# Performance work log

Hardware: AMD Instinct MI355X
Metric: run time of the kernel (lower is better)

Reference implementation:

```python
import jax, jax.numpy as jnp
import numpy as np

T, N, F_IN, H, E, OUT = 24, 20000, 64, 256, 320000, 1


def setup_inputs() -> dict:
    key = jax.random.key(0)
    ks = jax.random.split(key, 16)
    inp = {
        "x": jax.random.normal(ks[0], (T, N, F_IN), dtype=jnp.float32),
        "edge_index": jax.random.randint(ks[1], (2, E), 0, N, dtype=jnp.int32),
        "edge_weight": jax.random.uniform(ks[2], (E,), dtype=jnp.float32),
        # GCNConv 1 (input_size -> hidden)
        "W1": jax.random.normal(ks[3], (F_IN, H), dtype=jnp.float32) / np.sqrt(F_IN),
        "b1": jnp.zeros((H,), dtype=jnp.float32),
        # GCNConv 2 (hidden -> hidden)
        "W2": jax.random.normal(ks[4], (H, H), dtype=jnp.float32) / np.sqrt(H),
        "b2": jnp.zeros((H,), dtype=jnp.float32),
        # LayerNorm affine
        "ln_w": jnp.ones((H,), dtype=jnp.float32),
        "ln_b": jnp.zeros((H,), dtype=jnp.float32),
        # GRU (1 layer): weight_ih [3H,H_in], weight_hh [3H,H]
        "Wih": jax.random.normal(ks[5], (3 * H, H), dtype=jnp.float32) / np.sqrt(H),
        "Whh": jax.random.normal(ks[6], (3 * H, H), dtype=jnp.float32) / np.sqrt(H),
        "bih": jnp.zeros((3 * H,), dtype=jnp.float32),
        "bhh": jnp.zeros((3 * H,), dtype=jnp.float32),
        # fc
        "Wfc": jax.random.normal(ks[7], (OUT, H), dtype=jnp.float32) / np.sqrt(H),
        "bfc": jnp.zeros((OUT,), dtype=jnp.float32),
    }
    return inp


def _gcn_norm(edge_index, edge_weight, n_nodes):
    # PyG gcn_norm with self-loops (fill=1.0) and symmetric normalization.
    loop = jnp.arange(n_nodes, dtype=edge_index.dtype)
    src = jnp.concatenate([edge_index[0], loop])
    dst = jnp.concatenate([edge_index[1], loop])
    ew = jnp.concatenate([edge_weight, jnp.ones((n_nodes,), edge_weight.dtype)])
    deg = jax.ops.segment_sum(ew, dst, num_segments=n_nodes)
    dinv = jnp.where(deg > 0, jax.lax.rsqrt(deg), 0.0)
    norm = dinv[src] * ew * dinv[dst]
    return src, dst, norm


def _gcn_conv(x, src, dst, norm, W, b, n_nodes):
    h = x @ W                              # [N, out]
    msg = norm[:, None] * h[src]           # [E+N, out]
    out = jax.ops.segment_sum(msg, dst, num_segments=n_nodes)
    return out + b


def reference(x, edge_index, edge_weight, W1, b1, W2, b2, ln_w, ln_b,
              Wih, Whh, bih, bhh, Wfc, bfc):
    n_nodes = x.shape[1]
    src, dst, norm = _gcn_norm(edge_index, edge_weight, n_nodes)

    def encode(xt):  # xt: [N, F_IN]
        h = _gcn_conv(xt, src, dst, norm, W1, b1, n_nodes)
        h = jnp.where(h >= 0, h, 0.01 * h)  # leaky_relu, slope 0.01
        h = _gcn_conv(h, src, dst, norm, W2, b2, n_nodes)
        mu = jnp.mean(h, axis=-1, keepdims=True)
        var = jnp.mean(jnp.square(h - mu), axis=-1, keepdims=True)
        return (h - mu) * jax.lax.rsqrt(var + 1e-5) * ln_w + ln_b

    seq = jax.vmap(encode)(x)  # [T, N, H]

    def gru_step(h, xt):
        gi = xt @ Wih.T + bih
        gh = h @ Whh.T + bhh
        ir, iz, inn = jnp.split(gi, 3, axis=-1)
        hr, hz, hn = jnp.split(gh, 3, axis=-1)
        r = jax.nn.sigmoid(ir + hr)
        z = jax.nn.sigmoid(iz + hz)
        n = jnp.tanh(inn + r * hn)
        h_new = (1.0 - z) * n + z * h
        return h_new, None

    h0 = jnp.zeros((n_nodes, Whh.shape[1]), dtype=x.dtype)
    h_last, _ = jax.lax.scan(gru_step, h0, seq)
    return h_last @ Wfc.T + bfc  # [N, OUT]
```

## Files before the change

kernel.cpp:

```cpp
#include <hip/hip_runtime.h>
#include <math.h>

#define T_STEPS 24
#define N_NODES 20000
#define F_IN 64
#define H_DIM 256
#define H3 (3 * H_DIM)
#define TC 4
#define NCHUNK (T_STEPS / TC)

using f16x8 = __attribute__((ext_vector_type(8))) _Float16;
using f16x4 = __attribute__((ext_vector_type(4))) _Float16;
using f16x2 = __attribute__((ext_vector_type(2))) _Float16;
using f32x4 = __attribute__((ext_vector_type(4))) float;

__device__ __forceinline__ void gload_lds16(const void* g, void* l) {
    __builtin_amdgcn_global_load_lds(
        (const __attribute__((address_space(1))) void*)(uintptr_t)g,
        (__attribute__((address_space(3))) void*)l, 16, 0, 0);
}

__device__ __forceinline__ float sigmoidf_(float x) { return 1.0f / (1.0f + expf(-x)); }

__global__ void init_deg_kernel(float* deg, int* indeg, int n) {
    int i = blockIdx.x * blockDim.x + threadIdx.x;
    if (i < n) { deg[i] = 1.0f; indeg[i] = 0; }
}

__global__ void accum_deg_kernel(const int* __restrict__ src, const int* __restrict__ dst,
                                 const float* __restrict__ ew, float* deg, int* indeg, int E) {
    int e = blockIdx.x * blockDim.x + threadIdx.x;
    if (e < E) {
        atomicAdd(&deg[dst[e]], ew[e]);
        atomicAdd(&indeg[dst[e]], 1);
    }
}

__global__ void dinv_kernel(float* deg, float* selfnorm, int n) {
    int i = blockIdx.x * blockDim.x + threadIdx.x;
    if (i < n) {
        float d = deg[i];
        float di = (d > 0.0f) ? rsqrtf(d) : 0.0f;
        deg[i] = di;
        selfnorm[i] = di * di;
    }
}

__global__ void edge_norm_kernel(const int* __restrict__ src, const int* __restrict__ dst,
                                 const float* __restrict__ ew, const float* __restrict__ dinv,
                                 float* norm, int E) {
    int e = blockIdx.x * blockDim.x + threadIdx.x;
    if (e < E) norm[e] = dinv[src[e]] * ew[e] * dinv[dst[e]];
}

__global__ void scan_kernel(const int* __restrict__ indeg, int* offs, int* cursor, int N) {
    __shared__ int part[1024];
    int t = threadIdx.x;
    const int CH = (N + 1023) / 1024;
    int s = 0;
    for (int i = 0; i < CH; i++) {
        int idx = t * CH + i;
        if (idx < N) s += indeg[idx];
    }
    part[t] = s;
    __syncthreads();
    for (int off = 1; off < 1024; off <<= 1) {
        int v = (t >= off) ? part[t - off] : 0;
        __syncthreads();
        part[t] += v;
        __syncthreads();
    }
    int base = (t == 0) ? 0 : part[t - 1];
    for (int i = 0; i < CH; i++) {
        int idx = t * CH + i;
        if (idx < N) {
            offs[idx] = base;
            cursor[idx] = base;
            base += indeg[idx];
        }
    }
    if (t == 0) offs[N] = part[1023];
}

__global__ void csr_fill_kernel(const int* __restrict__ src, const int* __restrict__ dst,
                                const float* __restrict__ norm, int* cursor,
                                int* csr_src, float* csr_norm, int E) {
    int e = blockIdx.x * blockDim.x + threadIdx.x;
    if (e < E) {
        int d = dst[e];
        int pos = atomicAdd(&cursor[d], 1);
        csr_src[pos] = src[e];
        csr_norm[pos] = norm[e];
    }
}

__global__ void pack_b16_kernel(const float* __restrict__ W, _Float16* __restrict__ P,
                                int K, int Nn, int trans) {
    int idx = blockIdx.x * blockDim.x + threadIdx.x;
    int total = (K >> 3) * Nn;
    if (idx >= total) return;
    int kk = idx / Nn, c = idx - kk * Nn;
    int n = c;
    if (trans == 2) {
        int a = c / 48, w = c % 48;
        int g = w >> 4, b = w & 15;
        n = g * 256 + a * 16 + b;
    }
    size_t o = (size_t)idx * 8;
    for (int j = 0; j < 8; ++j) {
        float v = (trans != 0) ? W[(size_t)n * K + kk * 8 + j] : W[(size_t)(kk * 8 + j) * Nn + n];
        P[o + j] = (_Float16)v;
    }
}

__global__ void perm_bias_kernel(const float* __restrict__ b, float* __restrict__ pb) {
    int c = blockIdx.x * blockDim.x + threadIdx.x;
    if (c < H3) {
        int a = c / 48, w = c % 48;
        int g = w >> 4, bb = w & 15;
        pb[c] = b[g * 256 + a * 16 + bb];
    }
}

__global__ void agg1_kernel(const float* __restrict__ xs, const int* __restrict__ offs,
                            const int* __restrict__ csr_src, const float* __restrict__ csr_norm,
                            const float* __restrict__ selfnorm,
                            _Float16* __restrict__ out, int N) {
    int t = blockIdx.y;
    int n = blockIdx.x * 4 + (threadIdx.x >> 6);
    int lane = threadIdx.x & 63;
    int fg = lane & 15, ep = lane >> 4;
    const float* xsl = xs + (size_t)t * N * F_IN;
    f32x4 acc = (f32x4){0.f, 0.f, 0.f, 0.f};
    int e0 = offs[n], e1 = offs[n + 1];
    int e = e0 + ep;
    for (; e + 4 < e1; e += 8) {
        int sA = csr_src[e], sB = csr_src[e + 4];
        float wA = csr_norm[e], wB = csr_norm[e + 4];
        f32x4 vA = *(const f32x4*)&xsl[(size_t)sA * F_IN + fg * 4];
        f32x4 vB = *(const f32x4*)&xsl[(size_t)sB * F_IN + fg * 4];
#pragma unroll
        for (int c = 0; c < 4; ++c) acc[c] = fmaf(wA, vA[c], acc[c]);
#pragma unroll
        for (int c = 0; c < 4; ++c) acc[c] = fmaf(wB, vB[c], acc[c]);
    }
    if (e < e1) {
        int s = csr_src[e];
        float w = csr_norm[e];
        f32x4 v = *(const f32x4*)&xsl[(size_t)s * F_IN + fg * 4];
#pragma unroll
        for (int c = 0; c < 4; ++c) acc[c] = fmaf(w, v[c], acc[c]);
    }
#pragma unroll
    for (int c = 0; c < 4; ++c) {
        acc[c] += __shfl_xor(acc[c], 16, 64);
        acc[c] += __shfl_xor(acc[c], 32, 64);
    }
    f32x4 own = *(const f32x4*)&xsl[(size_t)n * F_IN + fg * 4];
    float sn = selfnorm[n];
#pragma unroll
    for (int c = 0; c < 4; ++c) acc[c] = fmaf(sn, own[c], acc[c]);
    if (ep == 0) {
        f16x4 o = { (_Float16)acc[0], (_Float16)acc[1], (_Float16)acc[2], (_Float16)acc[3] };
        *(f16x4*)&out[((size_t)t * N + n) * F_IN + fg * 4] = o;
    }
}

__global__ void agg2_kernel(const _Float16* __restrict__ hs, const int* __restrict__ offs,
                            const int* __restrict__ csr_src, const float* __restrict__ csr_norm,
                            const float* __restrict__ selfnorm,
                            _Float16* __restrict__ out, int N) {
    int t = blockIdx.y;
    int n = blockIdx.x * 4 + (threadIdx.x >> 6);
    int lane = threadIdx.x & 63;
    const _Float16* hsl = hs + (size_t)t * N * H_DIM;
    f16x4 own = *(const f16x4*)&hsl[(size_t)n * H_DIM + lane * 4];
    float sn = selfnorm[n];
    f32x4 acc;
#pragma unroll
    for (int c = 0; c < 4; ++c) acc[c] = sn * (float)own[c];
    int e0 = offs[n], e1 = offs[n + 1];
    int e = e0;
    for (; e + 4 <= e1; e += 4) {
        int s0 = csr_src[e], s1 = csr_src[e + 1], s2 = csr_src[e + 2], s3 = csr_src[e + 3];
        float w0 = csr_norm[e], w1 = csr_norm[e + 1], w2 = csr_norm[e + 2], w3 = csr_norm[e + 3];
        f16x4 v0 = *(const f16x4*)&hsl[(size_t)s0 * H_DIM + lane * 4];
        f16x4 v1 = *(const f16x4*)&hsl[(size_t)s1 * H_DIM + lane * 4];
        f16x4 v2 = *(const f16x4*)&hsl[(size_t)s2 * H_DIM + lane * 4];
        f16x4 v3 = *(const f16x4*)&hsl[(size_t)s3 * H_DIM + lane * 4];
#pragma unroll
        for (int c = 0; c < 4; ++c) acc[c] = fmaf(w0, (float)v0[c], acc[c]);
#pragma unroll
        for (int c = 0; c < 4; ++c) acc[c] = fmaf(w1, (float)v1[c], acc[c]);
#pragma unroll
        for (int c = 0; c < 4; ++c) acc[c] = fmaf(w2, (float)v2[c], acc[c]);
#pragma unroll
        for (int c = 0; c < 4; ++c) acc[c] = fmaf(w3, (float)v3[c], acc[c]);
    }
    for (; e < e1; ++e) {
        int s = csr_src[e];
        float w = csr_norm[e];
        f16x4 v = *(const f16x4*)&hsl[(size_t)s * H_DIM + lane * 4];
#pragma unroll
        for (int c = 0; c < 4; ++c) acc[c] = fmaf(w, (float)v[c], acc[c]);
    }
    f16x4 o = { (_Float16)acc[0], (_Float16)acc[1], (_Float16)acc[2], (_Float16)acc[3] };
    *(f16x4*)&out[((size_t)t * N + n) * H_DIM + lane * 4] = o;
}

__global__ __launch_bounds__(256, 4)
void conv1_kernel(const _Float16* __restrict__ A, const _Float16* __restrict__ Bp,
                  const float* __restrict__ bias, _Float16* __restrict__ C16,
                  int M, int Nn, int K) {
    __shared__ _Float16 As[4][128][8];
    __shared__ _Float16 Bs[4][128][8];

    const int tid = threadIdx.x;
    const int wave = tid >> 6, lane = tid & 63;
    const int bm = blockIdx.x * 128, bn = blockIdx.y * 128;
    const int wm = (wave >> 1) * 64, wn = (wave & 1) * 64;
    const int kq = lane >> 4, r = lane & 15;

    f32x4 acc[4][4];
#pragma unroll
    for (int i = 0; i < 4; ++i)
#pragma unroll
        for (int j = 0; j < 4; ++j) acc[i][j] = (f32x4){0.f, 0.f, 0.f, 0.f};

    for (int k0 = 0; k0 < K; k0 += 32) {
        __syncthreads();
        const int kb = k0 >> 3;
#pragma unroll
        for (int it = 0; it < 2; ++it) {
            int c = it * 256 + tid;
            int kk = c >> 7, idx = c & 127;
            int row = bm + idx;
            if (row >= M) row = M - 1;
            size_t aoff = (size_t)row * K + k0 + kk * 8;
            size_t boff = ((size_t)(kb + kk) * Nn + bn + idx) * 8;
            gload_lds16(A + aoff, &As[0][0][0] + (size_t)c * 8);
            gload_lds16(Bp + boff, &Bs[0][0][0] + (size_t)c * 8);
        }
        __syncthreads();

        f16x8 a[4], b[4];
#pragma unroll
        for (int f = 0; f < 4; ++f) {
            a[f] = *(const f16x8*)&As[kq][wm + f * 16 + r][0];
            b[f] = *(const f16x8*)&Bs[kq][wn + f * 16 + r][0];
        }
#pragma unroll
        for (int i = 0; i < 4; ++i)
#pragma unroll
            for (int j = 0; j < 4; ++j)
                acc[i][j] = __builtin_amdgcn_mfma_f32_16x16x32_f16(a[i], b[j], acc[i][j], 0, 0, 0);
    }

#pragma unroll
    for (int j = 0; j < 4; ++j) {
        int col = bn + wn + j * 16 + r;
        float bv = bias[col];
#pragma unroll
        for (int i = 0; i < 4; ++i) {
#pragma unroll
            for (int q = 0; q < 4; ++q) {
                int row = bm + wm + i * 16 + kq * 4 + q;
                if (row < M) {
                    float v = acc[i][j][q] + bv;
                    v = (v >= 0.0f) ? v : 0.01f * v;
                    C16[(size_t)row * Nn + col] = (_Float16)v;
                }
            }
        }
    }
}

__global__ __launch_bounds__(256, 2)
void conv2ln_kernel(const _Float16* __restrict__ A, const _Float16* __restrict__ Bp,
                    const float* __restrict__ b2, const float* __restrict__ lnw,
                    const float* __restrict__ lnb, _Float16* __restrict__ out, int M) {
    __shared__ _Float16 As[4][128][8];
    __shared__ _Float16 Bs[4][256][8];
    __shared__ float lnP[128][2][2];

    const int tid = threadIdx.x;
    const int wave = tid >> 6, lane = tid & 63;
    const int bm = blockIdx.x * 128;
    const int wm = (wave >> 1) * 64, wn = (wave & 1) * 128;
    const int cw = wave & 1;
    const int kq = lane >> 4, r = lane & 15;

    f32x4 acc[4][8];
#pragma unroll
    for (int i = 0; i < 4; ++i)
#pragma unroll
        for (int j = 0; j < 8; ++j) acc[i][j] = (f32x4){0.f, 0.f, 0.f, 0.f};

    for (int k0 = 0; k0 < H_DIM; k0 += 32) {
        __syncthreads();
        const int kb = k0 >> 3;
#pragma unroll
        for (int it = 0; it < 2; ++it) {
            int c = it * 256 + tid;
            int kk = c >> 7, idx = c & 127;
            int row = bm + idx;
            if (row >= M) row = M - 1;
            gload_lds16(A + (size_t)row * H_DIM + k0 + kk * 8, &As[0][0][0] + (size_t)c * 8);
        }
#pragma unroll
        for (int it = 0; it < 4; ++it) {
            int c = it * 256 + tid;
            int kk = c >> 8, col = c & 255;
            gload_lds16(Bp + ((size_t)(kb + kk) * H_DIM + col) * 8, &Bs[0][0][0] + (size_t)c * 8);
        }
        __syncthreads();

        f16x8 a[4], b[8];
#pragma unroll
        for (int f = 0; f < 4; ++f) a[f] = *(const f16x8*)&As[kq][wm + f * 16 + r][0];
#pragma unroll
        for (int f = 0; f < 8; ++f) b[f] = *(const f16x8*)&Bs[kq][wn + f * 16 + r][0];
#pragma unroll
        for (int i = 0; i < 4; ++i)
#pragma unroll
            for (int j = 0; j < 8; ++j)
                acc[i][j] = __builtin_amdgcn_mfma_f32_16x16x32_f16(a[i], b[j], acc[i][j], 0, 0, 0);
    }

#pragma unroll
    for (int i = 0; i < 4; ++i) {
#pragma unroll
        for (int q = 0; q < 4; ++q) {
            float s = 0.f, s2 = 0.f;
#pragma unroll
            for (int j = 0; j < 8; ++j) {
                float v = acc[i][j][q] + b2[wn + j * 16 + r];
                acc[i][j][q] = v;
                s += v;
                s2 += v * v;
            }
#pragma unroll
            for (int m = 1; m < 16; m <<= 1) {
                s += __shfl_xor(s, m, 64);
                s2 += __shfl_xor(s2, m, 64);
            }
            int lrow = wm + i * 16 + kq * 4 + q;
            if (r == 0) { lnP[lrow][cw][0] = s; lnP[lrow][cw][1] = s2; }
        }
    }
    __syncthreads();

#pragma unroll
    for (int i = 0; i < 4; ++i) {
#pragma unroll
        for (int q = 0; q < 4; ++q) {
            int lrow = wm + i * 16 + kq * 4 + q;
            int row = bm + lrow;
            float S = lnP[lrow][0][0] + lnP[lrow][1][0];
            float S2 = lnP[lrow][0][1] + lnP[lrow][1][1];
            float mu = S * (1.0f / H_DIM);
            float var = S2 * (1.0f / H_DIM) - mu * mu;
            float rstd = rsqrtf(var + 1e-5f);
            if (row < M) {
#pragma unroll
                for (int j = 0; j < 8; ++j) {
                    int col = wn + j * 16 + r;
                    float o = (acc[i][j][q] - mu) * rstd * lnw[col] + lnb[col];
                    out[(size_t)row * H_DIM + col] = (_Float16)o;
                }
            }
        }
    }
}

__global__ __launch_bounds__(256, 2)
void gru_step_kernel(const _Float16* __restrict__ hprev, const _Float16* __restrict__ e,
                     const _Float16* __restrict__ Bhh, const _Float16* __restrict__ Bih,
                     const float* __restrict__ pbhh, const float* __restrict__ pbih,
                     _Float16* __restrict__ hnew, int M) {
    __shared__ _Float16 Ah[4][128][8];
    __shared__ _Float16 Ae[4][128][8];
    __shared__ _Float16 Bsh[4][96][8];
    __shared__ _Float16 Bsi[4][96][8];

    const int tid = threadIdx.x;
    const int wave = tid >> 6, lane = tid & 63;
    const int bm = blockIdx.y * 128, bn = blockIdx.x * 96;
    const int wm = (wave >> 1) * 64, wn = (wave & 1) * 48;
    const int kq = lane >> 4, r = lane & 15;

    f32x4 arz[4][2], ahn[4], ainn[4];
#pragma unroll
    for (int i = 0; i < 4; ++i) {
        arz[i][0] = (f32x4){0.f, 0.f, 0.f, 0.f};
        arz[i][1] = (f32x4){0.f, 0.f, 0.f, 0.f};
        ahn[i] = (f32x4){0.f, 0.f, 0.f, 0.f};
        ainn[i] = (f32x4){0.f, 0.f, 0.f, 0.f};
    }

    for (int k0 = 0; k0 < H_DIM; k0 += 32) {
        __syncthreads();
        const int kb = k0 >> 3;
#pragma unroll
        for (int it = 0; it < 2; ++it) {
            int c = it * 256 + tid;
            int kk = c >> 7, idx = c & 127;
            int row = bm + idx;
            if (row >= M) row = M - 1;
            size_t ao = (size_t)row * H_DIM + k0 + kk * 8;
            gload_lds16(hprev + ao, &Ah[0][0][0] + (size_t)c * 8);
            gload_lds16(e + ao, &Ae[0][0][0] + (size_t)c * 8);
        }
        {
            int c = tid;
            int kk = c / 96, col = c - kk * 96;
            size_t bo = ((size_t)(kb + kk) * H3 + bn + col) * 8;
            gload_lds16(Bhh + bo, &Bsh[0][0][0] + (size_t)c * 8);
            gload_lds16(Bih + bo, &Bsi[0][0][0] + (size_t)c * 8);
            if (tid < 128) {
                int c2 = 256 + tid;
                int kk2 = c2 / 96, col2 = c2 - kk2 * 96;
                size_t bo2 = ((size_t)(kb + kk2) * H3 + bn + col2) * 8;
                gload_lds16(Bhh + bo2, &Bsh[0][0][0] + (size_t)c2 * 8);
                gload_lds16(Bih + bo2, &Bsi[0][0][0] + (size_t)c2 * 8);
            }
        }
        __syncthreads();

        f16x8 ah[4], ae[4], bh[3], bi[3];
#pragma unroll
        for (int f = 0; f < 4; ++f) {
            ah[f] = *(const f16x8*)&Ah[kq][wm + f * 16 + r][0];
            ae[f] = *(const f16x8*)&Ae[kq][wm + f * 16 + r][0];
        }
#pragma unroll
        for (int f = 0; f < 3; ++f) {
            bh[f] = *(const f16x8*)&Bsh[kq][wn + f * 16 + r][0];
            bi[f] = *(const f16x8*)&Bsi[kq][wn + f * 16 + r][0];
        }
#pragma unroll
        for (int i = 0; i < 4; ++i) {
            arz[i][0] = __builtin_amdgcn_mfma_f32_16x16x32_f16(ah[i], bh[0], arz[i][0], 0, 0, 0);
            arz[i][0] = __builtin_amdgcn_mfma_f32_16x16x32_f16(ae[i], bi[0], arz[i][0], 0, 0, 0);
            arz[i][1] = __builtin_amdgcn_mfma_f32_16x16x32_f16(ah[i], bh[1], arz[i][1], 0, 0, 0);
            arz[i][1] = __builtin_amdgcn_mfma_f32_16x16x32_f16(ae[i], bi[1], arz[i][1], 0, 0, 0);
            ahn[i] = __builtin_amdgcn_mfma_f32_16x16x32_f16(ah[i], bh[2], ahn[i], 0, 0, 0);
            ainn[i] = __builtin_amdgcn_mfma_f32_16x16x32_f16(ae[i], bi[2], ainn[i], 0, 0, 0);
        }
    }

    const int colbase = bn + wn;
    const int agrp = colbase / 48;
    const int f = agrp * 16 + r;
    const float b_r = pbhh[colbase + r] + pbih[colbase + r];
    const float b_z = pbhh[colbase + 16 + r] + pbih[colbase + 16 + r];
    const float b_hn = pbhh[colbase + 32 + r];
    const float b_in = pbih[colbase + 32 + r];
#pragma unroll
    for (int i = 0; i < 4; ++i) {
#pragma unroll
        for (int q = 0; q < 4; ++q) {
            int row = bm + wm + i * 16 + kq * 4 + q;
            if (row < M) {
                float rg = sigmoidf_(arz[i][0][q] + b_r);
                float zg = sigmoidf_(arz[i][1][q] + b_z);
                float nn = tanhf(ainn[i][q] + b_in + rg * (ahn[i][q] + b_hn));
                float hp = (float)hprev[(size_t)row * H_DIM + f];
                hnew[(size_t)row * H_DIM + f] = (_Float16)((1.0f - zg) * nn + zg * hp);
            }
        }
    }
}

__global__ void fc_kernel(const _Float16* __restrict__ h, const float* __restrict__ Wfc,
                          const float* __restrict__ bfc, float* __restrict__ out, int N) {
    int n = blockIdx.x * 4 + (threadIdx.x >> 6);
    int lane = threadIdx.x & 63;
    if (n >= N) return;
    f16x4 hv = *(const f16x4*)&h[(size_t)n * H_DIM + lane * 4];
    float4 wv = *(const float4*)&Wfc[lane * 4];
    float acc = (float)hv[0] * wv.x + (float)hv[1] * wv.y + (float)hv[2] * wv.z + (float)hv[3] * wv.w;
#pragma unroll
    for (int o = 32; o > 0; o >>= 1) acc += __shfl_down(acc, o, 64);
    if (lane == 0) out[n] = acc + bfc[0];
}

extern "C" void kernel_launch(void* const* d_in, const int* in_sizes, int n_in,
                              void* d_out, int out_size, void* d_ws, size_t ws_size,
                              hipStream_t stream) {
    const float* x   = (const float*)d_in[0];
    const int* eidx  = (const int*)d_in[1];
    const float* ew  = (const float*)d_in[2];
    const float* W1  = (const float*)d_in[3];
    const float* b1  = (const float*)d_in[4];
    const float* W2  = (const float*)d_in[5];
    const float* b2  = (const float*)d_in[6];
    const float* lnw = (const float*)d_in[7];
    const float* lnb = (const float*)d_in[8];
    const float* Wih = (const float*)d_in[9];
    const float* Whh = (const float*)d_in[10];
    const float* bih = (const float*)d_in[11];
    const float* bhh = (const float*)d_in[12];
    const float* Wfc = (const float*)d_in[13];
    const float* bfc = (const float*)d_in[14];

    const int E = in_sizes[2];
    const int N = N_NODES;
    const int* src = eidx;
    const int* dst = eidx + E;

    uintptr_t p = (uintptr_t)d_ws;
    auto alloc = [&](size_t bytes) -> void* {
        p = (p + 255) & ~(uintptr_t)255;
        void* r = (void*)p;
        p += bytes;
        return r;
    };
    float* deg      = (float*)alloc(N * sizeof(float));
    float* selfnorm = (float*)alloc(N * sizeof(float));
    float* norm     = (float*)alloc(E * sizeof(float));
    int* indeg      = (int*)alloc(N * sizeof(int));
    int* offs       = (int*)alloc((N + 1) * sizeof(int));
    int* cursor     = (int*)alloc(N * sizeof(int));
    int* csr_src    = (int*)alloc(E * sizeof(int));
    float* csr_norm = (float*)alloc(E * sizeof(float));
    _Float16* W1p   = (_Float16*)alloc((size_t)F_IN * H_DIM * sizeof(_Float16));
    _Float16* W2p   = (_Float16*)alloc((size_t)H_DIM * H_DIM * sizeof(_Float16));
    _Float16* Wihp  = (_Float16*)alloc((size_t)H_DIM * H3 * sizeof(_Float16));
    _Float16* Whhp  = (_Float16*)alloc((size_t)H_DIM * H3 * sizeof(_Float16));
    float* pbih     = (float*)alloc(H3 * sizeof(float));
    float* pbhh     = (float*)alloc(H3 * sizeof(float));
    _Float16* a1_16 = (_Float16*)alloc((size_t)TC * N * F_IN * sizeof(_Float16));
    _Float16* h1_16 = (_Float16*)alloc((size_t)TC * N * H_DIM * sizeof(_Float16));
    _Float16* a2_16 = (_Float16*)alloc((size_t)TC * N * H_DIM * sizeof(_Float16));
    _Float16* e16   = (_Float16*)alloc((size_t)TC * N * H_DIM * sizeof(_Float16));
    _Float16* h_a   = (_Float16*)alloc((size_t)N * H_DIM * sizeof(_Float16));
    _Float16* h_b   = (_Float16*)alloc((size_t)N * H_DIM * sizeof(_Float16));

    const int TB = 256;
    hipLaunchKernelGGL(init_deg_kernel, dim3((N + TB - 1) / TB), dim3(TB), 0, stream, deg, indeg, N);
    hipLaunchKernelGGL(accum_deg_kernel, dim3((E + TB - 1) / TB), dim3(TB), 0, stream, src, dst, ew, deg, indeg, E);
    hipLaunchKernelGGL(dinv_kernel, dim3((N + TB - 1) / TB), dim3(TB), 0, stream, deg, selfnorm, N);
    hipLaunchKernelGGL(edge_norm_kernel, dim3((E + TB - 1) / TB), dim3(TB), 0, stream, src, dst, ew, deg, norm, E);
    hipLaunchKernelGGL(scan_kernel, dim3(1), dim3(1024), 0, stream, indeg, offs, cursor, N);
    hipLaunchKernelGGL(csr_fill_kernel, dim3((E + TB - 1) / TB), dim3(TB), 0, stream, src, dst, norm, cursor, csr_src, csr_norm, E);

    {
        int tot = (F_IN / 8) * H_DIM;
        hipLaunchKernelGGL(pack_b16_kernel, dim3((tot + TB - 1) / TB), dim3(TB), 0, stream, W1, W1p, F_IN, H_DIM, 0);
        tot = (H_DIM / 8) * H_DIM;
        hipLaunchKernelGGL(pack_b16_kernel, dim3((tot + TB - 1) / TB), dim3(TB), 0, stream, W2, W2p, H_DIM, H_DIM, 0);
        tot = (H_DIM / 8) * H3;
        hipLaunchKernelGGL(pack_b16_kernel, dim3((tot + TB - 1) / TB), dim3(TB), 0, stream, Wih, Wihp, H_DIM, H3, 2);
        hipLaunchKernelGGL(pack_b16_kernel, dim3((tot + TB - 1) / TB), dim3(TB), 0, stream, Whh, Whhp, H_DIM, H3, 2);
        hipLaunchKernelGGL(perm_bias_kernel, dim3((H3 + TB - 1) / TB), dim3(TB), 0, stream, bih, pbih);
        hipLaunchKernelGGL(perm_bias_kernel, dim3((H3 + TB - 1) / TB), dim3(TB), 0, stream, bhh, pbhh);
    }

    hipMemsetAsync(h_a, 0, (size_t)N * H_DIM * sizeof(_Float16), stream);

    const int MC = TC * N;
    dim3 gb(256);
    dim3 g_conv1(MC / 128, H_DIM / 128);
    dim3 g_c2ln(MC / 128);
    dim3 g_gru(8, (N + 127) / 128);
    dim3 g_agg(N / 4, TC);

    _Float16* h_cur = h_a;
    _Float16* h_nxt = h_b;

    for (int chunk = 0; chunk < NCHUNK; ++chunk) {
        const float* xc = x + (size_t)chunk * TC * N * F_IN;
        hipLaunchKernelGGL(agg1_kernel, g_agg, dim3(256), 0, stream,
                           xc, offs, csr_src, csr_norm, selfnorm, a1_16, N);
        hipLaunchKernelGGL(conv1_kernel, g_conv1, gb, 0, stream,
                           a1_16, W1p, b1, h1_16, MC, H_DIM, F_IN);
        hipLaunchKernelGGL(agg2_kernel, g_agg, dim3(256), 0, stream,
                           h1_16, offs, csr_src, csr_norm, selfnorm, a2_16, N);
        hipLaunchKernelGGL(conv2ln_kernel, g_c2ln, gb, 0, stream,
                           a2_16, W2p, b2, lnw, lnb, e16, MC);
        for (int tc = 0; tc < TC; ++tc) {
            hipLaunchKernelGGL(gru_step_kernel, g_gru, gb, 0, stream,
                               h_cur, e16 + (size_t)tc * N * H_DIM, Whhp, Wihp,
                               pbhh, pbih, h_nxt, N);
            _Float16* tmp = h_cur; h_cur = h_nxt; h_nxt = tmp;
        }
    }

    hipLaunchKernelGGL(fc_kernel, dim3((N + 3) / 4), dim3(256), 0, stream, h_cur, Wfc, bfc, (float*)d_out, N);
}
```

Before: 2.609 ms.

## Convert input to fp16 before aggregation and widen gather loads to 16 bytes

A new kernel converts each chunk of x to fp16 before the first graph aggregation. That aggregation now gathers 8-half vectors with 8 edges in flight per wave instead of 4-float vectors. The second aggregation splits each wave into two halves that process alternate edges with 16-byte loads, then reduces them with a lane shuffle. The GRU step kernel's launch bounds request 3 blocks per SM instead of 2. These changes aim to cut gather bandwidth and raise memory-level parallelism, at the cost of an extra conversion pass, fp16 rounding of inputs, and possible register pressure in the GRU kernel.

```diff
diff --git a/kernel.cpp b/kernel.cpp
--- a/kernel.cpp
+++ b/kernel.cpp
@@ -122,47 +122,59 @@
     }
 }
 
-__global__ void agg1_kernel(const float* __restrict__ xs, const int* __restrict__ offs,
+__global__ void tofp16_kernel(const float* __restrict__ in, _Float16* __restrict__ out, int n4) {
+    int i = blockIdx.x * blockDim.x + threadIdx.x;
+    if (i < n4) {
+        float4 v = ((const float4*)in)[i];
+        f16x4 o = { (_Float16)v.x, (_Float16)v.y, (_Float16)v.z, (_Float16)v.w };
+        ((f16x4*)out)[i] = o;
+    }
+}
+
+__global__ void agg1_kernel(const _Float16* __restrict__ xs, const int* __restrict__ offs,
                             const int* __restrict__ csr_src, const float* __restrict__ csr_norm,
                             const float* __restrict__ selfnorm,
                             _Float16* __restrict__ out, int N) {
     int t = blockIdx.y;
     int n = blockIdx.x * 4 + (threadIdx.x >> 6);
     int lane = threadIdx.x & 63;
-    int fg = lane & 15, ep = lane >> 4;
-    const float* xsl = xs + (size_t)t * N * F_IN;
-    f32x4 acc = (f32x4){0.f, 0.f, 0.f, 0.f};
+    int fg = lane & 7, ep = lane >> 3;
+    const _Float16* xsl = xs + (size_t)t * N * F_IN;
+    float acc[8] = {};
     int e0 = offs[n], e1 = offs[n + 1];
     int e = e0 + ep;
-    for (; e + 4 < e1; e += 8) {
-        int sA = csr_src[e], sB = csr_src[e + 4];
-        float wA = csr_norm[e], wB = csr_norm[e + 4];
-        f32x4 vA = *(const f32x4*)&xsl[(size_t)sA * F_IN + fg * 4];
-        f32x4 vB = *(const f32x4*)&xsl[(size_t)sB * F_IN + fg * 4];
-#pragma unroll
-        for (int c = 0; c < 4; ++c) acc[c] = fmaf(wA, vA[c], acc[c]);
-#pragma unroll
-        for (int c = 0; c < 4; ++c) acc[c] = fmaf(wB, vB[c], acc[c]);
+    for (; e + 8 < e1; e += 16) {
+        int sA = csr_src[e], sB = csr_src[e + 8];
+        float wA = csr_norm[e], wB = csr_norm[e + 8];
+        f16x8 vA = *(const f16x8*)&xsl[(size_t)sA * F_IN + fg * 8];
+        f16x8 vB = *(const f16x8*)&xsl[(size_t)sB * F_IN + fg * 8];
+#pragma unroll
+        for (int c = 0; c < 8; ++c) acc[c] = fmaf(wA, (float)vA[c], acc[c]);
+#pragma unroll
+        for (int c = 0; c < 8; ++c) acc[c] = fmaf(wB, (float)vB[c], acc[c]);
     }
     if (e < e1) {
         int s = csr_src[e];
         float w = csr_norm[e];
-        f32x4 v = *(const f32x4*)&xsl[(size_t)s * F_IN + fg * 4];
-#pragma unroll
-        for (int c = 0; c < 4; ++c) acc[c] = fmaf(w, v[c], acc[c]);
-    }
-#pragma unroll
-    for (int c = 0; c < 4; ++c) {
+        f16x8 v = *(const f16x8*)&xsl[(size_t)s * F_IN + fg * 8];
+#pragma unroll
+        for (int c = 0; c < 8; ++c) acc[c] = fmaf(w, (float)v[c], acc[c]);
+    }
+#pragma unroll
+    for (int c = 0; c < 8; ++c) {
+        acc[c] += __shfl_xor(acc[c], 8, 64);
         acc[c] += __shfl_xor(acc[c], 16, 64);
         acc[c] += __shfl_xor(acc[c], 32, 64);
     }
-    f32x4 own = *(const f32x4*)&xsl[(size_t)n * F_IN + fg * 4];
+    f16x8 own = *(const f16x8*)&xsl[(size_t)n * F_IN + fg * 8];
     float sn = selfnorm[n];
 #pragma unroll
-    for (int c = 0; c < 4; ++c) acc[c] = fmaf(sn, own[c], acc[c]);
+    for (int c = 0; c < 8; ++c) acc[c] = fmaf(sn, (float)own[c], acc[c]);
     if (ep == 0) {
-        f16x4 o = { (_Float16)acc[0], (_Float16)acc[1], (_Float16)acc[2], (_Float16)acc[3] };
-        *(f16x4*)&out[((size_t)t * N + n) * F_IN + fg * 4] = o;
+        f16x8 o;
+#pragma unroll
+        for (int c = 0; c < 8; ++c) o[c] = (_Float16)acc[c];
+        *(f16x8*)&out[((size_t)t * N + n) * F_IN + fg * 8] = o;
     }
 }
 
@@ -173,39 +185,40 @@
     int t = blockIdx.y;
     int n = blockIdx.x * 4 + (threadIdx.x >> 6);
     int lane = threadIdx.x & 63;
+    int half = lane >> 5, fl = lane & 31;
     const _Float16* hsl = hs + (size_t)t * N * H_DIM;
-    f16x4 own = *(const f16x4*)&hsl[(size_t)n * H_DIM + lane * 4];
-    float sn = selfnorm[n];
-    f32x4 acc;
-#pragma unroll
-    for (int c = 0; c < 4; ++c) acc[c] = sn * (float)own[c];
+    float acc[8] = {};
     int e0 = offs[n], e1 = offs[n + 1];
-    int e = e0;
-    for (; e + 4 <= e1; e += 4) {
-        int s0 = csr_src[e], s1 = csr_src[e + 1], s2 = csr_src[e + 2], s3 = csr_src[e + 3];
-        float w0 = csr_norm[e], w1 = csr_norm[e + 1], w2 = csr_norm[e + 2], w3 = csr_norm[e + 3];
-        f16x4 v0 = *(const f16x4*)&hsl[(size_t)s0 * H_DIM + lane * 4];
-        f16x4 v1 = *(const f16x4*)&hsl[(size_t)s1 * H_DIM + lane * 4];
-        f16x4 v2 = *(const f16x4*)&hsl[(size_t)s2 * H_DIM + lane * 4];
-        f16x4 v3 = *(const f16x4*)&hsl[(size_t)s3 * H_DIM + lane * 4];
-#pragma unroll
-        for (int c = 0; c < 4; ++c) acc[c] = fmaf(w0, (float)v0[c], acc[c]);
-#pragma unroll
-        for (int c = 0; c < 4; ++c) acc[c] = fmaf(w1, (float)v1[c], acc[c]);
-#pragma unroll
-        for (int c = 0; c < 4; ++c) acc[c] = fmaf(w2, (float)v2[c], acc[c]);
-#pragma unroll
-        for (int c = 0; c < 4; ++c) acc[c] = fmaf(w3, (float)v3[c], acc[c]);
-    }
-    for (; e < e1; ++e) {
+    int e = e0 + half;
+    for (; e + 2 < e1; e += 4) {
+        int sA = csr_src[e], sB = csr_src[e + 2];
+        float wA = csr_norm[e], wB = csr_norm[e + 2];
+        f16x8 vA = *(const f16x8*)&hsl[(size_t)sA * H_DIM + fl * 8];
+        f16x8 vB = *(const f16x8*)&hsl[(size_t)sB * H_DIM + fl * 8];
+#pragma unroll
+        for (int c = 0; c < 8; ++c) acc[c] = fmaf(wA, (float)vA[c], acc[c]);
+#pragma unroll
+        for (int c = 0; c < 8; ++c) acc[c] = fmaf(wB, (float)vB[c], acc[c]);
+    }
+    if (e < e1) {
         int s = csr_src[e];
         float w = csr_norm[e];
-        f16x4 v = *(const f16x4*)&hsl[(size_t)s * H_DIM + lane * 4];
-#pragma unroll
-        for (int c = 0; c < 4; ++c) acc[c] = fmaf(w, (float)v[c], acc[c]);
-    }
-    f16x4 o = { (_Float16)acc[0], (_Float16)acc[1], (_Float16)acc[2], (_Float16)acc[3] };
-    *(f16x4*)&out[((size_t)t * N + n) * H_DIM + lane * 4] = o;
+        f16x8 v = *(const f16x8*)&hsl[(size_t)s * H_DIM + fl * 8];
+#pragma unroll
+        for (int c = 0; c < 8; ++c) acc[c] = fmaf(w, (float)v[c], acc[c]);
+    }
+#pragma unroll
+    for (int c = 0; c < 8; ++c) acc[c] += __shfl_xor(acc[c], 32, 64);
+    f16x8 own = *(const f16x8*)&hsl[(size_t)n * H_DIM + fl * 8];
+    float sn = selfnorm[n];
+#pragma unroll
+    for (int c = 0; c < 8; ++c) acc[c] = fmaf(sn, (float)own[c], acc[c]);
+    if (half == 0) {
+        f16x8 o;
+#pragma unroll
+        for (int c = 0; c < 8; ++c) o[c] = (_Float16)acc[c];
+        *(f16x8*)&out[((size_t)t * N + n) * H_DIM + fl * 8] = o;
+    }
 }
 
 __global__ __launch_bounds__(256, 4)
@@ -373,7 +386,7 @@
     }
 }
 
-__global__ __launch_bounds__(256, 2)
+__global__ __launch_bounds__(256, 3)
 void gru_step_kernel(const _Float16* __restrict__ hprev, const _Float16* __restrict__ e,
                      const _Float16* __restrict__ Bhh, const _Float16* __restrict__ Bih,
                      const float* __restrict__ pbhh, const float* __restrict__ pbih,
@@ -530,6 +543,7 @@
     _Float16* Whhp  = (_Float16*)alloc((size_t)H_DIM * H3 * sizeof(_Float16));
     float* pbih     = (float*)alloc(H3 * sizeof(float));
     float* pbhh     = (float*)alloc(H3 * sizeof(float));
+    _Float16* xs16  = (_Float16*)alloc((size_t)TC * N * F_IN * sizeof(_Float16));
     _Float16* a1_16 = (_Float16*)alloc((size_t)TC * N * F_IN * sizeof(_Float16));
     _Float16* h1_16 = (_Float16*)alloc((size_t)TC * N * H_DIM * sizeof(_Float16));
     _Float16* a2_16 = (_Float16*)alloc((size_t)TC * N * H_DIM * sizeof(_Float16));
@@ -571,8 +585,10 @@
 
     for (int chunk = 0; chunk < NCHUNK; ++chunk) {
         const float* xc = x + (size_t)chunk * TC * N * F_IN;
+        int n4 = TC * N * F_IN / 4;
+        hipLaunchKernelGGL(tofp16_kernel, dim3((n4 + TB - 1) / TB), dim3(TB), 0, stream, xc, xs16, n4);
         hipLaunchKernelGGL(agg1_kernel, g_agg, dim3(256), 0, stream,
-                           xc, offs, csr_src, csr_norm, selfnorm, a1_16, N);
+                           xs16, offs, csr_src, csr_norm, selfnorm, a1_16, N);
         hipLaunchKernelGGL(conv1_kernel, g_conv1, gb, 0, stream,
                            a1_16, W1p, b1, h1_16, MC, H_DIM, F_IN);
         hipLaunchKernelGGL(agg2_kernel, g_agg, dim3(256), 0, stream,
```

Result: no change. 2.580 ms (-1.1%).
